# Optimization experiments

Measured on AMD Instinct MI355X. Metric: run time of the kernel, lower is better.

Reference implementation:

```python
import jax, jax.numpy as jnp
import numpy as np

ATOM = 34
HID = 256
LATENT = 128
CELLS = 512
B, N = 64, 128
NEG = -9e15


def setup_inputs() -> dict:
    key = jax.random.key(0)
    ks = jax.random.split(key, 20)
    inp = {}
    inp["xs"] = jax.random.normal(ks[0], (B, N, ATOM), dtype=jnp.float32)
    inp["A"] = jax.random.randint(ks[1], (B, N, N), 0, 2, dtype=jnp.int32)
    inp["cell_emb"] = jax.random.normal(ks[2], (B, CELLS), dtype=jnp.float32)
    inp["Wg"] = jax.random.normal(ks[3], (3, ATOM, ATOM), dtype=jnp.float32) * 0.17
    inp["bg"] = jnp.zeros((3, ATOM), dtype=jnp.float32)
    inp["attn"] = jax.random.normal(ks[4], (3, 2 * ATOM), dtype=jnp.float32) * 0.17
    # W_gnn_trans: 34 -> 256
    inp["Wt"] = jax.random.normal(ks[5], (ATOM, HID), dtype=jnp.float32) * 0.08
    inp["bt"] = jnp.zeros((HID,), dtype=jnp.float32)
    # ffn: 256 -> 34 ; ffn2: 34 -> latent
    inp["Wf"] = jax.random.normal(ks[6], (HID, ATOM), dtype=jnp.float32) * 0.08
    inp["bf"] = jnp.zeros((ATOM,), dtype=jnp.float32)
    inp["Wf2"] = jax.random.normal(ks[7], (ATOM, LATENT), dtype=jnp.float32) * 0.11
    inp["bf2"] = jnp.zeros((LATENT,), dtype=jnp.float32)
    # Decoder MLP: (latent+cells)->128->256->512->1
    din = LATENT + CELLS
    inp["W1"] = jax.random.normal(ks[8], (din, 128), dtype=jnp.float32) * 0.05
    inp["b1"] = jnp.zeros((128,), dtype=jnp.float32)
    inp["W2"] = jax.random.normal(ks[9], (128, 256), dtype=jnp.float32) * 0.07
    inp["b2"] = jnp.zeros((256,), dtype=jnp.float32)
    inp["W3"] = jax.random.normal(ks[10], (256, 512), dtype=jnp.float32) * 0.05
    inp["b3"] = jnp.zeros((512,), dtype=jnp.float32)
    inp["W4"] = jax.random.normal(ks[11], (512, 1), dtype=jnp.float32) * 0.06
    inp["b4"] = jnp.zeros((1,), dtype=jnp.float32)
    return inp


def reference(xs, A, cell_emb, Wg, bg, attn, Wt, bt, Wf, bf, Wf2, bf2,
              W1, b1, W2, b2, W3, b3, W4, b4):
    # ---- gnn(): 3 rounds of GAT-style masked-softmax message passing ----
    # a_input[b,p,q] = [h[b,p], h[b,q]], so e = leaky_relu(h@a1 outer+ h@a2)
    h0 = xs
    mask = A > 0  # [B,N,N]
    x = xs
    for i in range(3):
        h = jax.nn.relu(jnp.einsum('bnd,de->bne', x, Wg[i]) + bg[i])  # [B,N,34]
        f_src = h @ attn[i, :ATOM]   # [B,N] -- score contribution of row atom
        f_dst = h @ attn[i, ATOM:]   # [B,N] -- score contribution of col atom
        e = jax.nn.leaky_relu(f_src[:, :, None] + f_dst[:, None, :], 0.01)
        scores = jnp.where(mask, e, NEG)
        att = jax.nn.softmax(scores, axis=2)  # dropout disabled (deterministic)
        x = x + jnp.einsum('bpq,bqd->bpd', att, h)
    g = jax.nn.relu(jnp.einsum('bnd,dh->bnh', x, Wt) + bt)  # [B,N,HID]

    # ---- VEC_forward ----
    d = jnp.einsum('bnh,hd->bnd', g, Wf) + bf + h0        # ffn + residual to input xs
    d = jnp.einsum('bnd,dl->bnl', d, Wf2) + bf2           # [B,N,LATENT]
    d = jnp.max(d, axis=1)                                # [B,LATENT]
    vec = jax.nn.sigmoid(jnp.concatenate([d, cell_emb], axis=-1))

    # ---- Decoder_mlp (dropout disabled) ----
    hminus = jax.nn.relu(vec @ W1 + b1)
    hminus = jax.nn.relu(hminus @ W2 + b2)
    hminus = jax.nn.relu(hminus @ W3 + b3)
    score = hminus @ W4 + b4                              # [B,1]
    return score
```

## Files before the change

### kernel.cpp

```cpp
#include <hip/hip_runtime.h>

constexpr int ATOM = 34;
constexpr int HID = 256;
constexpr int LATENT = 128;
constexpr int CELLS = 512;
constexpr int NN = 128;
constexpr int NA = NN * ATOM;
#define NEGF (-9e15f)

__global__ __launch_bounds__(512) void k_gat(
    const float* __restrict__ xsrc, const int* __restrict__ A,
    const float* __restrict__ Wg, const float* __restrict__ bg,
    const float* __restrict__ av, float* __restrict__ X)
{
    const int b = blockIdx.x >> 2, q4 = blockIdx.x & 3;
    const int t = threadIdx.x, lane = t & 63, wave = t >> 6;
    const int p0 = q4 * 32;

    __shared__ float xl[NN][36];
    __shared__ float hlT[ATOM][132];
    __shared__ float att[32][NN];
    __shared__ float wg[ATOM * ATOM];
    __shared__ float fs[NN], fd[NN];
    __shared__ float bgs[ATOM], avs[2 * ATOM];

    for (int i = t; i < ATOM * ATOM; i += 512) wg[i] = Wg[i];
    if (t < ATOM)     bgs[t] = bg[t];
    if (t < 2 * ATOM) avs[t] = av[t];
    const float* xp = xsrc + b * NA;
    for (int i = t; i < NA; i += 512) xl[i / ATOM][i % ATOM] = xp[i];
    __syncthreads();

    {
        const int n = t >> 2, sub = t & 3;
        float xr[36];
        float4* xr4 = (float4*)xr;
        const float4* xlr = (const float4*)&xl[n][0];
        #pragma unroll
        for (int k = 0; k < 9; ++k) xr4[k] = xlr[k];
        for (int e = sub; e < ATOM; e += 4) {
            float acc = bgs[e];
            #pragma unroll
            for (int d = 0; d < ATOM; ++d) acc += xr[d] * wg[d * ATOM + e];
            hlT[e][n] = fmaxf(acc, 0.f);
        }
    }
    __syncthreads();

    if (t < 2 * NN) {
        const int n = t & (NN - 1), w = t >> 7;
        const float* avp = avs + w * ATOM;
        float acc = 0.f;
        #pragma unroll
        for (int d = 0; d < ATOM; ++d) acc += hlT[d][n] * avp[d];
        if (w == 0) fs[n] = acc; else fd[n] = acc;
    }
    __syncthreads();

    const int* Ab = A + b * NN * NN;
    #pragma unroll
    for (int i = 0; i < 4; ++i) {
        int lp = wave * 4 + i, gp = p0 + lp;
        float fsv = fs[gp];
        unsigned long long m0 = __ballot(Ab[gp * NN + lane] > 0);
        unsigned long long m1 = __ballot(Ab[gp * NN + 64 + lane] > 0);
        float s0 = fsv + fd[lane];
        s0 = (s0 > 0.f) ? s0 : 0.01f * s0;
        if (!((m0 >> lane) & 1ull)) s0 = NEGF;
        float s1 = fsv + fd[64 + lane];
        s1 = (s1 > 0.f) ? s1 : 0.01f * s1;
        if (!((m1 >> lane) & 1ull)) s1 = NEGF;
        float mx = fmaxf(s0, s1);
        #pragma unroll
        for (int o = 32; o >= 1; o >>= 1) mx = fmaxf(mx, __shfl_xor(mx, o, 64));
        float e0 = __expf(s0 - mx), e1 = __expf(s1 - mx);
        float sm = e0 + e1;
        #pragma unroll
        for (int o = 32; o >= 1; o >>= 1) sm += __shfl_xor(sm, o, 64);
        float inv = 1.f / sm;
        att[lp][lane]      = e0 * inv;
        att[lp][64 + lane] = e1 * inv;
    }
    __syncthreads();

    {
        const int p = t >> 4, g = t & 15;
        const float4* ap  = (const float4*)&att[p][0];
        const float4* h1p = (const float4*)&hlT[g][0];
        const float4* h2p = (const float4*)&hlT[g + 16][0];
        float a1 = 0.f, a2 = 0.f;
        #pragma unroll 8
        for (int k = 0; k < 32; ++k) {
            float4 a4 = ap[k], x1 = h1p[k], x2 = h2p[k];
            a1 += a4.x * x1.x + a4.y * x1.y + a4.z * x1.z + a4.w * x1.w;
            a2 += a4.x * x2.x + a4.y * x2.y + a4.z * x2.z + a4.w * x2.w;
        }
        const int gp = p0 + p;
        float* Xr = X + b * NA + gp * ATOM;
        Xr[g]      = xl[gp][g] + a1;
        Xr[g + 16] = xl[gp][g + 16] + a2;
        if (g < 2) {
            const float4* h3p = (const float4*)&hlT[g + 32][0];
            float a3 = 0.f;
            #pragma unroll 8
            for (int k = 0; k < 32; ++k) {
                float4 a4 = ap[k], x3 = h3p[k];
                a3 += a4.x * x3.x + a4.y * x3.y + a4.z * x3.z + a4.w * x3.w;
            }
            Xr[g + 32] = xl[gp][g + 32] + a3;
        }
    }
}

__global__ __launch_bounds__(512) void k_phaseB(
    const float* __restrict__ X, const float* __restrict__ xs,
    const float* __restrict__ Wt, const float* __restrict__ bt,
    const float* __restrict__ Wf, const float* __restrict__ bf,
    const float* __restrict__ Wf2, const float* __restrict__ bf2,
    float* __restrict__ DM)
{
    const int b = blockIdx.x >> 2, q4 = blockIdx.x & 3;
    const int t = threadIdx.x;
    const int p0 = q4 * 32;
    __shared__ float wt[HID * 36];
    __shared__ float wf[HID * 36];
    __shared__ float xl[32][36];
    __shared__ float dlT[ATOM][33];
    __shared__ float wf2s[ATOM * LATENT];
    __shared__ float bts[HID];
    __shared__ float bfs[ATOM];
    __shared__ float sl[512];

    for (int i = t; i < ATOM * HID; i += 512) {
        int d = i >> 8, h = i & 255;
        wt[h * 36 + d] = Wt[i];
    }
    for (int i = t; i < HID * ATOM; i += 512) {
        int h = i / ATOM, j = i % ATOM;
        wf[h * 36 + j] = Wf[i];
    }
    for (int i = t; i < ATOM * LATENT; i += 512) wf2s[i] = Wf2[i];
    if (t < HID)  bts[t] = bt[t];
    if (t < ATOM) bfs[t] = bf[t];
    for (int i = t; i < 32 * ATOM; i += 512) xl[i / ATOM][i % ATOM] = X[b * NA + p0 * ATOM + i];
    __syncthreads();

    const int row = t & 31, sub = t >> 5;
    float dp[ATOM];
    #pragma unroll
    for (int j = 0; j < ATOM; ++j) dp[j] = 0.f;
    {
        float xr[36];
        float4* xr4 = (float4*)xr;
        const float4* xlr = (const float4*)&xl[row][0];
        #pragma unroll
        for (int k = 0; k < 9; ++k) xr4[k] = xlr[k];
        for (int i = 0; i < 16; ++i) {
            const int h = sub + 16 * i;
            float acc = bts[h];
            const float4* wtp = (const float4*)&wt[h * 36];
            #pragma unroll
            for (int k = 0; k < 8; ++k) {
                float4 w4 = wtp[k];
                acc += xr[4*k] * w4.x + xr[4*k+1] * w4.y + xr[4*k+2] * w4.z + xr[4*k+3] * w4.w;
            }
            acc += xr[32] * wt[h * 36 + 32] + xr[33] * wt[h * 36 + 33];
            acc = fmaxf(acc, 0.f);
            const float4* wfp = (const float4*)&wf[h * 36];
            #pragma unroll
            for (int k = 0; k < 8; ++k) {
                float4 w4 = wfp[k];
                dp[4*k]   += acc * w4.x; dp[4*k+1] += acc * w4.y;
                dp[4*k+2] += acc * w4.z; dp[4*k+3] += acc * w4.w;
            }
            dp[32] += acc * wf[h * 36 + 32];
            dp[33] += acc * wf[h * 36 + 33];
        }
    }
    __syncthreads();
    {
        float* pl = (sub < 8) ? wt : wf;
        const int s8 = sub & 7;
        #pragma unroll
        for (int j = 0; j < ATOM; ++j) pl[(s8 * 32 + row) * ATOM + j] = dp[j];
    }
    __syncthreads();
    for (int i = t; i < 32 * ATOM; i += 512) {
        int rr = i / ATOM, j = i % ATOM;
        float dv = bfs[j] + xs[b * NA + (p0 + rr) * ATOM + j];
        #pragma unroll
        for (int s = 0; s < 8; ++s)
            dv += wt[(s * 32 + rr) * ATOM + j] + wf[(s * 32 + rr) * ATOM + j];
        dlT[j][rr] = dv;
    }
    __syncthreads();
    {
        const int l = t & 127, chunk = t >> 7;
        float w2r[ATOM];
        #pragma unroll
        for (int j = 0; j < ATOM; ++j) w2r[j] = wf2s[j * LATENT + l];
        float mx = -3.4e38f;
        for (int rr = chunk * 8; rr < chunk * 8 + 8; ++rr) {
            float acc = bf2[l];
            #pragma unroll
            for (int j = 0; j < ATOM; ++j) acc += dlT[j][rr] * w2r[j];
            mx = fmaxf(mx, acc);
        }
        sl[chunk * 128 + l] = mx;
    }
    __syncthreads();
    if (t < LATENT)
        DM[(b * 4 + q4) * LATENT + t] =
            fmaxf(fmaxf(sl[t], sl[128 + t]), fmaxf(sl[256 + t], sl[384 + t]));
}

__global__ __launch_bounds__(1024) void k_dec(
    const float* __restrict__ DM, const float* __restrict__ cell,
    const float* __restrict__ W1, const float* __restrict__ b1,
    const float* __restrict__ W2, const float* __restrict__ b2,
    const float* __restrict__ W3, const float* __restrict__ b3,
    const float* __restrict__ W4, const float* __restrict__ b4,
    float* __restrict__ out)
{
    const int b = blockIdx.x, t = threadIdx.x, lane = t & 63, wave = t >> 6;
    __shared__ float vec[LATENT + CELLS];
    __shared__ float h1[128], h2[256], h3[512];
    __shared__ float sl[1024];
    if (t < LATENT) {
        float m = fmaxf(fmaxf(DM[(b*4+0)*LATENT + t], DM[(b*4+1)*LATENT + t]),
                        fmaxf(DM[(b*4+2)*LATENT + t], DM[(b*4+3)*LATENT + t]));
        vec[t] = 1.f / (1.f + __expf(-m));
    } else if (t >= 512) {
        int c = t - 512;
        vec[LATENT + c] = 1.f / (1.f + __expf(-cell[b * CELLS + c]));
    }
    __syncthreads();
    {
        const int j = t & 127, part = t >> 7;
        float acc = 0.f;
        #pragma unroll 4
        for (int k = part * 80; k < part * 80 + 80; ++k)
            acc += vec[k] * W1[k * 128 + j];
        sl[part * 128 + j] = acc;
    }
    __syncthreads();
    if (t < 128) {
        float v = b1[t];
        #pragma unroll
        for (int p = 0; p < 8; ++p) v += sl[p * 128 + t];
        h1[t] = fmaxf(v, 0.f);
    }
    __syncthreads();
    {
        const int j = t & 255, part = t >> 8;
        float acc = 0.f;
        #pragma unroll 4
        for (int k = part * 32; k < part * 32 + 32; ++k)
            acc += h1[k] * W2[k * 256 + j];
        sl[part * 256 + j] = acc;
    }
    __syncthreads();
    if (t < 256) h2[t] = fmaxf(sl[t] + sl[256 + t] + sl[512 + t] + sl[768 + t] + b2[t], 0.f);
    __syncthreads();
    {
        const int j = t & 511, part = t >> 9;
        float acc = 0.f;
        #pragma unroll 4
        for (int k = part * 128; k < part * 128 + 128; ++k)
            acc += h2[k] * W3[k * 512 + j];
        sl[part * 512 + j] = acc;
    }
    __syncthreads();
    if (t < 512) h3[t] = fmaxf(sl[t] + sl[512 + t] + b3[t], 0.f);
    __syncthreads();
    float v = (t < 512) ? h3[t] * W4[t] : 0.f;
    #pragma unroll
    for (int o = 32; o >= 1; o >>= 1) v += __shfl_xor(v, o, 64);
    if (lane == 0) sl[wave] = v;
    __syncthreads();
    if (t == 0) {
        float s = b4[0];
        #pragma unroll
        for (int w = 0; w < 16; ++w) s += sl[w];
        out[b] = s;
    }
}

extern "C" void kernel_launch(void* const* d_in, const int* in_sizes, int n_in,
                              void* d_out, int out_size, void* d_ws, size_t ws_size,
                              hipStream_t stream) {
    const float* xs       = (const float*)d_in[0];
    const int*   A        = (const int*)  d_in[1];
    const float* cell_emb = (const float*)d_in[2];
    const float* Wg       = (const float*)d_in[3];
    const float* bg       = (const float*)d_in[4];
    const float* attnv    = (const float*)d_in[5];
    const float* Wt       = (const float*)d_in[6];
    const float* bt       = (const float*)d_in[7];
    const float* Wf       = (const float*)d_in[8];
    const float* bf       = (const float*)d_in[9];
    const float* Wf2      = (const float*)d_in[10];
    const float* bf2      = (const float*)d_in[11];
    const float* W1       = (const float*)d_in[12];
    const float* b1       = (const float*)d_in[13];
    const float* W2       = (const float*)d_in[14];
    const float* b2       = (const float*)d_in[15];
    const float* W3       = (const float*)d_in[16];
    const float* b3       = (const float*)d_in[17];
    const float* W4       = (const float*)d_in[18];
    const float* b4       = (const float*)d_in[19];
    float* out = (float*)d_out;

    float* W  = (float*)d_ws;
    float* X0 = W;
    float* X1 = W + 278528;
    float* DM = W + 557056;

    k_gat<<<256, 512, 0, stream>>>(xs, A, Wg,                  bg,          attnv,          X0);
    k_gat<<<256, 512, 0, stream>>>(X0, A, Wg + ATOM * ATOM,    bg + ATOM,   attnv + 2*ATOM, X1);
    k_gat<<<256, 512, 0, stream>>>(X1, A, Wg + 2 * ATOM * ATOM, bg + 2*ATOM, attnv + 4*ATOM, X0);
    k_phaseB<<<256, 512, 0, stream>>>(X0, xs, Wt, bt, Wf, bf, Wf2, bf2, DM);
    k_dec<<<64, 1024, 0, stream>>>(DM, cell_emb, W1, b1, W2, b2, W3, b3, W4, b4, out);
}
```

Baseline: 178.6 us.

## Fuse phase-B FFN into last GAT layer and widen blocks to 1024 threads

Merges the post-GNN projection/FFN/max-pool kernel into the third GAT launch through a templated kernel, so the final node features stay in shared memory in a reused pool instead of being written to and re-read from global memory. It also removes one kernel launch. Block size grows from 512 to 1024 threads: the attention-weighted sum is split over two K-halves and combined with a shuffle, and the hidden-layer matmul splits the feature dimension in half. This doubles the threads per block and shares one shared-memory buffer across both phases. The cost is higher register and LDS pressure per block, which may lower occupancy.

Result: slower. 277.7 us (+55.5%).

```diff
diff --git a/kernel.cpp b/kernel.cpp
--- a/kernel.cpp
+++ b/kernel.cpp
@@ -8,42 +8,68 @@
 constexpr int NA = NN * ATOM;
 #define NEGF (-9e15f)
 
-__global__ __launch_bounds__(512) void k_gat(
+constexpr int POOL = 30848;
+
+template <bool FUSE_B>
+__global__ __launch_bounds__(1024) void k_gat(
     const float* __restrict__ xsrc, const int* __restrict__ A,
     const float* __restrict__ Wg, const float* __restrict__ bg,
-    const float* __restrict__ av, float* __restrict__ X)
+    const float* __restrict__ av, float* __restrict__ X,
+    const float* __restrict__ xs,
+    const float* __restrict__ Wt, const float* __restrict__ bt,
+    const float* __restrict__ Wf, const float* __restrict__ bf,
+    const float* __restrict__ Wf2, const float* __restrict__ bf2,
+    float* __restrict__ DM)
 {
+    __shared__ __align__(16) float pool[POOL];
     const int b = blockIdx.x >> 2, q4 = blockIdx.x & 3;
     const int t = threadIdx.x, lane = t & 63, wave = t >> 6;
     const int p0 = q4 * 32;
 
-    __shared__ float xl[NN][36];
-    __shared__ float hlT[ATOM][132];
-    __shared__ float att[32][NN];
-    __shared__ float wg[ATOM * ATOM];
-    __shared__ float fs[NN], fd[NN];
-    __shared__ float bgs[ATOM], avs[2 * ATOM];
-
-    for (int i = t; i < ATOM * ATOM; i += 512) wg[i] = Wg[i];
+    float* xl  = pool;
+    float* hlT = pool + 4608;
+    float* att = pool + 9096;
+    float* wgT = pool + 13192;
+    float* fs  = pool + 14416;
+    float* fd  = pool + 14544;
+    float* bgs = pool + 14672;
+    float* avs = pool + 14712;
+    float* xq  = pool + 29440;
+
+    for (int i = t; i < ATOM * ATOM; i += 1024) {
+        int d = i / ATOM, e = i - d * ATOM;
+        wgT[e * 36 + d] = Wg[i];
+    }
+    if (t < 68)  wgT[(t >> 1) * 36 + 34 + (t & 1)] = 0.f;
     if (t < ATOM)     bgs[t] = bg[t];
     if (t < 2 * ATOM) avs[t] = av[t];
     const float* xp = xsrc + b * NA;
-    for (int i = t; i < NA; i += 512) xl[i / ATOM][i % ATOM] = xp[i];
-    __syncthreads();
-
-    {
-        const int n = t >> 2, sub = t & 3;
+    for (int i = t; i < NA; i += 1024) xl[(i / ATOM) * 36 + (i % ATOM)] = xp[i];
+    if (t < 256) xl[(t >> 1) * 36 + 34 + (t & 1)] = 0.f;
+    __syncthreads();
+
+    {
+        const int n = t >> 3, sub = t & 7;
         float xr[36];
-        float4* xr4 = (float4*)xr;
-        const float4* xlr = (const float4*)&xl[n][0];
-        #pragma unroll
-        for (int k = 0; k < 9; ++k) xr4[k] = xlr[k];
-        for (int e = sub; e < ATOM; e += 4) {
+        {
+            float4* xr4 = (float4*)xr;
+            const float4* xlr = (const float4*)(xl + n * 36);
+            #pragma unroll
+            for (int k = 0; k < 9; ++k) xr4[k] = xlr[k];
+        }
+        auto hbody = [&](int e) {
             float acc = bgs[e];
-            #pragma unroll
-            for (int d = 0; d < ATOM; ++d) acc += xr[d] * wg[d * ATOM + e];
-            hlT[e][n] = fmaxf(acc, 0.f);
-        }
+            const float4* wp = (const float4*)(wgT + e * 36);
+            #pragma unroll
+            for (int k = 0; k < 9; ++k) {
+                float4 w4 = wp[k];
+                acc += xr[4*k] * w4.x + xr[4*k+1] * w4.y + xr[4*k+2] * w4.z + xr[4*k+3] * w4.w;
+            }
+            hlT[e * 132 + n] = fmaxf(acc, 0.f);
+        };
+        #pragma unroll
+        for (int j = 0; j < 4; ++j) hbody(sub + 8 * j);
+        if (sub < 2) hbody(sub + 32);
     }
     __syncthreads();
 
@@ -52,15 +78,15 @@
         const float* avp = avs + w * ATOM;
         float acc = 0.f;
         #pragma unroll
-        for (int d = 0; d < ATOM; ++d) acc += hlT[d][n] * avp[d];
+        for (int d = 0; d < ATOM; ++d) acc += hlT[d * 132 + n] * avp[d];
         if (w == 0) fs[n] = acc; else fd[n] = acc;
     }
     __syncthreads();
 
     const int* Ab = A + b * NN * NN;
     #pragma unroll
-    for (int i = 0; i < 4; ++i) {
-        int lp = wave * 4 + i, gp = p0 + lp;
+    for (int i = 0; i < 2; ++i) {
+        int lp = wave * 2 + i, gp = p0 + lp;
         float fsv = fs[gp];
         unsigned long long m0 = __ballot(Ab[gp * NN + lane] > 0);
         unsigned long long m1 = __ballot(Ab[gp * NN + 64 + lane] > 0);
@@ -78,140 +104,162 @@
         #pragma unroll
         for (int o = 32; o >= 1; o >>= 1) sm += __shfl_xor(sm, o, 64);
         float inv = 1.f / sm;
-        att[lp][lane]      = e0 * inv;
-        att[lp][64 + lane] = e1 * inv;
-    }
-    __syncthreads();
-
-    {
-        const int p = t >> 4, g = t & 15;
-        const float4* ap  = (const float4*)&att[p][0];
-        const float4* h1p = (const float4*)&hlT[g][0];
-        const float4* h2p = (const float4*)&hlT[g + 16][0];
-        float a1 = 0.f, a2 = 0.f;
-        #pragma unroll 8
-        for (int k = 0; k < 32; ++k) {
+        att[lp * NN + lane]      = e0 * inv;
+        att[lp * NN + 64 + lane] = e1 * inv;
+    }
+    __syncthreads();
+
+    {
+        const int p = t >> 5, g = t & 15, kh = (t >> 4) & 1;
+        const float4* ap  = (const float4*)(att + p * NN + kh * 64);
+        const float4* h1p = (const float4*)(hlT + g * 132 + kh * 64);
+        const float4* h2p = (const float4*)(hlT + (g + 16) * 132 + kh * 64);
+        float a1 = 0.f, a2 = 0.f, a3 = 0.f;
+        #pragma unroll
+        for (int k = 0; k < 16; ++k) {
             float4 a4 = ap[k], x1 = h1p[k], x2 = h2p[k];
             a1 += a4.x * x1.x + a4.y * x1.y + a4.z * x1.z + a4.w * x1.w;
             a2 += a4.x * x2.x + a4.y * x2.y + a4.z * x2.z + a4.w * x2.w;
         }
-        const int gp = p0 + p;
-        float* Xr = X + b * NA + gp * ATOM;
-        Xr[g]      = xl[gp][g] + a1;
-        Xr[g + 16] = xl[gp][g + 16] + a2;
         if (g < 2) {
-            const float4* h3p = (const float4*)&hlT[g + 32][0];
-            float a3 = 0.f;
-            #pragma unroll 8
-            for (int k = 0; k < 32; ++k) {
+            const float4* h3p = (const float4*)(hlT + (g + 32) * 132 + kh * 64);
+            #pragma unroll
+            for (int k = 0; k < 16; ++k) {
                 float4 a4 = ap[k], x3 = h3p[k];
                 a3 += a4.x * x3.x + a4.y * x3.y + a4.z * x3.z + a4.w * x3.w;
             }
-            Xr[g + 32] = xl[gp][g + 32] + a3;
-        }
-    }
-}
-
-__global__ __launch_bounds__(512) void k_phaseB(
-    const float* __restrict__ X, const float* __restrict__ xs,
-    const float* __restrict__ Wt, const float* __restrict__ bt,
-    const float* __restrict__ Wf, const float* __restrict__ bf,
-    const float* __restrict__ Wf2, const float* __restrict__ bf2,
-    float* __restrict__ DM)
-{
-    const int b = blockIdx.x >> 2, q4 = blockIdx.x & 3;
-    const int t = threadIdx.x;
-    const int p0 = q4 * 32;
-    __shared__ float wt[HID * 36];
-    __shared__ float wf[HID * 36];
-    __shared__ float xl[32][36];
-    __shared__ float dlT[ATOM][33];
-    __shared__ float wf2s[ATOM * LATENT];
-    __shared__ float bts[HID];
-    __shared__ float bfs[ATOM];
-    __shared__ float sl[512];
-
-    for (int i = t; i < ATOM * HID; i += 512) {
+        }
+        a1 += __shfl_xor(a1, 16, 64);
+        a2 += __shfl_xor(a2, 16, 64);
+        a3 += __shfl_xor(a3, 16, 64);
+        const int gp = p0 + p;
+        if (FUSE_B) {
+            if (kh == 0) {
+                xq[p * 44 + g] = xl[gp * 36 + g] + a1;
+                if (g < 2) xq[p * 44 + g + 32] = xl[gp * 36 + g + 32] + a3;
+            } else {
+                xq[p * 44 + g + 16] = xl[gp * 36 + g + 16] + a2;
+                if (g >= 6) xq[p * 44 + 28 + g] = 0.f;
+            }
+        } else {
+            float* Xr = X + b * NA + gp * ATOM;
+            if (kh == 0) {
+                Xr[g] = xl[gp * 36 + g] + a1;
+                if (g < 2) Xr[g + 32] = xl[gp * 36 + g + 32] + a3;
+            } else {
+                Xr[g + 16] = xl[gp * 36 + g + 16] + a2;
+            }
+        }
+    }
+
+    if (!FUSE_B) return;
+
+    __syncthreads();
+    float* wt   = pool;
+    float* wf   = pool + 11264;
+    float* wf2s = pool + 22528;
+    float* dlT  = pool + 26880;
+    float* sl   = pool + 28032;
+    float* bts  = pool + 29056;
+    float* bfs  = pool + 29312;
+
+    for (int i = t; i < ATOM * HID; i += 1024) {
         int d = i >> 8, h = i & 255;
-        wt[h * 36 + d] = Wt[i];
-    }
-    for (int i = t; i < HID * ATOM; i += 512) {
-        int h = i / ATOM, j = i % ATOM;
-        wf[h * 36 + j] = Wf[i];
-    }
-    for (int i = t; i < ATOM * LATENT; i += 512) wf2s[i] = Wf2[i];
+        wt[h * 44 + d] = Wt[i];
+    }
+    for (int i = t; i < HID * ATOM; i += 1024) {
+        int h = i / ATOM, j = i - h * ATOM;
+        wf[h * 44 + j] = Wf[i];
+    }
+    for (int i = t; i < 2560; i += 1024) {
+        int h = i / 10, c = 34 + i - (i / 10) * 10;
+        wt[h * 44 + c] = 0.f; wf[h * 44 + c] = 0.f;
+    }
+    for (int i = t; i < ATOM * LATENT; i += 1024) wf2s[i] = Wf2[i];
     if (t < HID)  bts[t] = bt[t];
     if (t < ATOM) bfs[t] = bf[t];
-    for (int i = t; i < 32 * ATOM; i += 512) xl[i / ATOM][i % ATOM] = X[b * NA + p0 * ATOM + i];
-    __syncthreads();
-
-    const int row = t & 31, sub = t >> 5;
-    float dp[ATOM];
-    #pragma unroll
-    for (int j = 0; j < ATOM; ++j) dp[j] = 0.f;
-    {
-        float xr[36];
-        float4* xr4 = (float4*)xr;
-        const float4* xlr = (const float4*)&xl[row][0];
-        #pragma unroll
-        for (int k = 0; k < 9; ++k) xr4[k] = xlr[k];
+    __syncthreads();
+
+    {
+        const int row = t >> 5, sub = t & 15, half = (t >> 4) & 1;
+        const int dbase = half * 20;
+        float xr[20];
+        {
+            const float4* xp4 = (const float4*)(xq + row * 44 + dbase);
+            float4* xr4 = (float4*)xr;
+            #pragma unroll
+            for (int k = 0; k < 5; ++k) xr4[k] = xp4[k];
+        }
+        float dp[20];
+        #pragma unroll
+        for (int j = 0; j < 20; ++j) dp[j] = 0.f;
+        #pragma unroll
         for (int i = 0; i < 16; ++i) {
             const int h = sub + 16 * i;
-            float acc = bts[h];
-            const float4* wtp = (const float4*)&wt[h * 36];
-            #pragma unroll
-            for (int k = 0; k < 8; ++k) {
+            float part = 0.f;
+            const float4* wtp = (const float4*)(wt + h * 44 + dbase);
+            #pragma unroll
+            for (int k = 0; k < 5; ++k) {
                 float4 w4 = wtp[k];
-                acc += xr[4*k] * w4.x + xr[4*k+1] * w4.y + xr[4*k+2] * w4.z + xr[4*k+3] * w4.w;
-            }
-            acc += xr[32] * wt[h * 36 + 32] + xr[33] * wt[h * 36 + 33];
-            acc = fmaxf(acc, 0.f);
-            const float4* wfp = (const float4*)&wf[h * 36];
-            #pragma unroll
-            for (int k = 0; k < 8; ++k) {
+                part += xr[4*k] * w4.x + xr[4*k+1] * w4.y + xr[4*k+2] * w4.z + xr[4*k+3] * w4.w;
+            }
+            float acc = fmaxf(part + __shfl_xor(part, 16, 64) + bts[h], 0.f);
+            const float4* wfp = (const float4*)(wf + h * 44 + dbase);
+            #pragma unroll
+            for (int k = 0; k < 5; ++k) {
                 float4 w4 = wfp[k];
                 dp[4*k]   += acc * w4.x; dp[4*k+1] += acc * w4.y;
                 dp[4*k+2] += acc * w4.z; dp[4*k+3] += acc * w4.w;
             }
-            dp[32] += acc * wf[h * 36 + 32];
-            dp[33] += acc * wf[h * 36 + 33];
-        }
-    }
-    __syncthreads();
-    {
-        float* pl = (sub < 8) ? wt : wf;
-        const int s8 = sub & 7;
-        #pragma unroll
-        for (int j = 0; j < ATOM; ++j) pl[(s8 * 32 + row) * ATOM + j] = dp[j];
-    }
-    __syncthreads();
-    for (int i = t; i < 32 * ATOM; i += 512) {
-        int rr = i / ATOM, j = i % ATOM;
-        float dv = bfs[j] + xs[b * NA + (p0 + rr) * ATOM + j];
+        }
+        __syncthreads();
+        {
+            const int s8 = sub & 7;
+            float* pl = (sub < 8) ? wt : wf;
+            const int jbase = half * 20;
+            #pragma unroll
+            for (int jj = 0; jj < 20; ++jj) {
+                int j = jbase + jj;
+                if (j < ATOM) pl[(s8 * 32 + row) * ATOM + j] = dp[jj];
+            }
+        }
+    }
+    __syncthreads();
+
+    const float* xsq = xs + b * NA + p0 * ATOM;
+    for (int i = t; i < 32 * ATOM; i += 1024) {
+        int rr = i / ATOM, j = i - rr * ATOM;
+        float dv = bfs[j] + xsq[rr * ATOM + j];
         #pragma unroll
         for (int s = 0; s < 8; ++s)
             dv += wt[(s * 32 + rr) * ATOM + j] + wf[(s * 32 + rr) * ATOM + j];
-        dlT[j][rr] = dv;
-    }
-    __syncthreads();
+        dlT[j * 33 + rr] = dv;
+    }
+    __syncthreads();
+
     {
         const int l = t & 127, chunk = t >> 7;
         float w2r[ATOM];
         #pragma unroll
         for (int j = 0; j < ATOM; ++j) w2r[j] = wf2s[j * LATENT + l];
+        const float bb = bf2[l];
         float mx = -3.4e38f;
-        for (int rr = chunk * 8; rr < chunk * 8 + 8; ++rr) {
-            float acc = bf2[l];
-            #pragma unroll
-            for (int j = 0; j < ATOM; ++j) acc += dlT[j][rr] * w2r[j];
+        #pragma unroll
+        for (int rr = 0; rr < 4; ++rr) {
+            float acc = bb;
+            #pragma unroll
+            for (int j = 0; j < ATOM; ++j) acc += dlT[j * 33 + chunk * 4 + rr] * w2r[j];
             mx = fmaxf(mx, acc);
         }
         sl[chunk * 128 + l] = mx;
     }
     __syncthreads();
-    if (t < LATENT)
-        DM[(b * 4 + q4) * LATENT + t] =
-            fmaxf(fmaxf(sl[t], sl[128 + t]), fmaxf(sl[256 + t], sl[384 + t]));
+    if (t < LATENT) {
+        float m = sl[t];
+        #pragma unroll
+        for (int s = 1; s < 8; ++s) m = fmaxf(m, sl[s * 128 + t]);
+        DM[(b * 4 + q4) * LATENT + t] = m;
+    }
 }
 
 __global__ __launch_bounds__(1024) void k_dec(
@@ -316,9 +364,11 @@
     float* X1 = W + 278528;
     float* DM = W + 557056;
 
-    k_gat<<<256, 512, 0, stream>>>(xs, A, Wg,                  bg,          attnv,          X0);
-    k_gat<<<256, 512, 0, stream>>>(X0, A, Wg + ATOM * ATOM,    bg + ATOM,   attnv + 2*ATOM, X1);
-    k_gat<<<256, 512, 0, stream>>>(X1, A, Wg + 2 * ATOM * ATOM, bg + 2*ATOM, attnv + 4*ATOM, X0);
-    k_phaseB<<<256, 512, 0, stream>>>(X0, xs, Wt, bt, Wf, bf, Wf2, bf2, DM);
+    k_gat<false><<<256, 1024, 0, stream>>>(xs, A, Wg, bg, attnv, X0,
+                                           xs, Wt, bt, Wf, bf, Wf2, bf2, DM);
+    k_gat<false><<<256, 1024, 0, stream>>>(X0, A, Wg + ATOM*ATOM, bg + ATOM, attnv + 2*ATOM, X1,
+                                           xs, Wt, bt, Wf, bf, Wf2, bf2, DM);
+    k_gat<true> <<<256, 1024, 0, stream>>>(X1, A, Wg + 2*ATOM*ATOM, bg + 2*ATOM, attnv + 4*ATOM, nullptr,
+                                           xs, Wt, bt, Wf, bf, Wf2, bf2, DM);
     k_dec<<<64, 1024, 0, stream>>>(DM, cell_emb, W1, b1, W2, b2, W3, b3, W4, b4, out);
 }
```

## Split GAT layers across 8 blocks per graph with transposed padded weights

Applied to the files above, without the earlier changes.

The GAT kernel now launches 512 blocks of 256 threads, each owning 16 target atoms instead of 32, so more blocks run concurrently across CUs. The Wg matrix is stored transposed and padded to 36 so the per-node linear layer can use float4 shared-memory reads, with 2 threads per node instead of 4. Launch bounds request 2 blocks per CU for both GAT and phaseB. In exchange, each block still recomputes the full 128-node hidden projection and attention logits, so that redundant work per graph doubles.

Result: no change. 177.8 us (-0.5%).

```diff
diff --git a/kernel.cpp b/kernel.cpp
--- a/kernel.cpp
+++ b/kernel.cpp
@@ -8,51 +8,63 @@
 constexpr int NA = NN * ATOM;
 #define NEGF (-9e15f)
 
-__global__ __launch_bounds__(512) void k_gat(
+__global__ __launch_bounds__(256, 2) void k_gat(
     const float* __restrict__ xsrc, const int* __restrict__ A,
     const float* __restrict__ Wg, const float* __restrict__ bg,
     const float* __restrict__ av, float* __restrict__ X)
 {
-    const int b = blockIdx.x >> 2, q4 = blockIdx.x & 3;
+    const int b = blockIdx.x >> 3, s8 = blockIdx.x & 7;
     const int t = threadIdx.x, lane = t & 63, wave = t >> 6;
-    const int p0 = q4 * 32;
-
-    __shared__ float xl[NN][36];
-    __shared__ float hlT[ATOM][132];
-    __shared__ float att[32][NN];
-    __shared__ float wg[ATOM * ATOM];
-    __shared__ float fs[NN], fd[NN];
-    __shared__ float bgs[ATOM], avs[2 * ATOM];
-
-    for (int i = t; i < ATOM * ATOM; i += 512) wg[i] = Wg[i];
+    const int p0 = s8 * 16;
+
+    __shared__ __align__(16) float xl[NN * 36];
+    __shared__ __align__(16) float hlT[ATOM * 132];
+    __shared__ __align__(16) float att[16 * NN];
+    __shared__ __align__(16) float wgT[ATOM * 36];
+    __shared__ float fs[NN], fd[NN], bgs[ATOM], avs[2 * ATOM];
+
+    for (int i = t; i < ATOM * ATOM; i += 256) {
+        int d = i / ATOM, e = i - d * ATOM;
+        wgT[e * 36 + d] = Wg[i];
+    }
+    if (t < 68)  wgT[(t >> 1) * 36 + 34 + (t & 1)] = 0.f;
     if (t < ATOM)     bgs[t] = bg[t];
     if (t < 2 * ATOM) avs[t] = av[t];
     const float* xp = xsrc + b * NA;
-    for (int i = t; i < NA; i += 512) xl[i / ATOM][i % ATOM] = xp[i];
-    __syncthreads();
-
-    {
-        const int n = t >> 2, sub = t & 3;
+    for (int i = t; i < NA; i += 256) xl[(i / ATOM) * 36 + (i % ATOM)] = xp[i];
+    xl[(t >> 1) * 36 + 34 + (t & 1)] = 0.f;
+    __syncthreads();
+
+    {
+        const int n = t >> 1, sub = t & 1;
         float xr[36];
-        float4* xr4 = (float4*)xr;
-        const float4* xlr = (const float4*)&xl[n][0];
-        #pragma unroll
-        for (int k = 0; k < 9; ++k) xr4[k] = xlr[k];
-        for (int e = sub; e < ATOM; e += 4) {
+        {
+            float4* xr4 = (float4*)xr;
+            const float4* p4 = (const float4*)(xl + n * 36);
+            #pragma unroll
+            for (int k = 0; k < 9; ++k) xr4[k] = p4[k];
+        }
+        #pragma unroll
+        for (int j = 0; j < 17; ++j) {
+            const int e = sub + 2 * j;
             float acc = bgs[e];
-            #pragma unroll
-            for (int d = 0; d < ATOM; ++d) acc += xr[d] * wg[d * ATOM + e];
-            hlT[e][n] = fmaxf(acc, 0.f);
-        }
-    }
-    __syncthreads();
-
-    if (t < 2 * NN) {
-        const int n = t & (NN - 1), w = t >> 7;
+            const float4* wp = (const float4*)(wgT + e * 36);
+            #pragma unroll
+            for (int k = 0; k < 9; ++k) {
+                float4 w = wp[k];
+                acc += xr[4*k] * w.x + xr[4*k+1] * w.y + xr[4*k+2] * w.z + xr[4*k+3] * w.w;
+            }
+            hlT[e * 132 + n] = fmaxf(acc, 0.f);
+        }
+    }
+    __syncthreads();
+
+    {
+        const int n = t & 127, w = t >> 7;
         const float* avp = avs + w * ATOM;
         float acc = 0.f;
         #pragma unroll
-        for (int d = 0; d < ATOM; ++d) acc += hlT[d][n] * avp[d];
+        for (int d = 0; d < ATOM; ++d) acc += hlT[d * 132 + n] * avp[d];
         if (w == 0) fs[n] = acc; else fd[n] = acc;
     }
     __syncthreads();
@@ -78,16 +90,16 @@
         #pragma unroll
         for (int o = 32; o >= 1; o >>= 1) sm += __shfl_xor(sm, o, 64);
         float inv = 1.f / sm;
-        att[lp][lane]      = e0 * inv;
-        att[lp][64 + lane] = e1 * inv;
-    }
-    __syncthreads();
-
-    {
-        const int p = t >> 4, g = t & 15;
-        const float4* ap  = (const float4*)&att[p][0];
-        const float4* h1p = (const float4*)&hlT[g][0];
-        const float4* h2p = (const float4*)&hlT[g + 16][0];
+        att[lp * NN + lane]      = e0 * inv;
+        att[lp * NN + 64 + lane] = e1 * inv;
+    }
+    __syncthreads();
+
+    {
+        const int p = t >> 4, g = t & 15, gp = p0 + p;
+        const float4* ap  = (const float4*)(att + p * NN);
+        const float4* h1p = (const float4*)(hlT + g * 132);
+        const float4* h2p = (const float4*)(hlT + (g + 16) * 132);
         float a1 = 0.f, a2 = 0.f;
         #pragma unroll 8
         for (int k = 0; k < 32; ++k) {
@@ -95,24 +107,23 @@
             a1 += a4.x * x1.x + a4.y * x1.y + a4.z * x1.z + a4.w * x1.w;
             a2 += a4.x * x2.x + a4.y * x2.y + a4.z * x2.z + a4.w * x2.w;
         }
-        const int gp = p0 + p;
         float* Xr = X + b * NA + gp * ATOM;
-        Xr[g]      = xl[gp][g] + a1;
-        Xr[g + 16] = xl[gp][g + 16] + a2;
+        Xr[g]      = xl[gp * 36 + g] + a1;
+        Xr[g + 16] = xl[gp * 36 + g + 16] + a2;
         if (g < 2) {
-            const float4* h3p = (const float4*)&hlT[g + 32][0];
+            const float4* h3p = (const float4*)(hlT + (g + 32) * 132);
             float a3 = 0.f;
             #pragma unroll 8
             for (int k = 0; k < 32; ++k) {
                 float4 a4 = ap[k], x3 = h3p[k];
                 a3 += a4.x * x3.x + a4.y * x3.y + a4.z * x3.z + a4.w * x3.w;
             }
-            Xr[g + 32] = xl[gp][g + 32] + a3;
+            Xr[g + 32] = xl[gp * 36 + g + 32] + a3;
         }
     }
 }
 
-__global__ __launch_bounds__(512) void k_phaseB(
+__global__ __launch_bounds__(512, 2) void k_phaseB(
     const float* __restrict__ X, const float* __restrict__ xs,
     const float* __restrict__ Wt, const float* __restrict__ bt,
     const float* __restrict__ Wf, const float* __restrict__ bf,
@@ -316,9 +327,9 @@
     float* X1 = W + 278528;
     float* DM = W + 557056;
 
-    k_gat<<<256, 512, 0, stream>>>(xs, A, Wg,                  bg,          attnv,          X0);
-    k_gat<<<256, 512, 0, stream>>>(X0, A, Wg + ATOM * ATOM,    bg + ATOM,   attnv + 2*ATOM, X1);
-    k_gat<<<256, 512, 0, stream>>>(X1, A, Wg + 2 * ATOM * ATOM, bg + 2*ATOM, attnv + 4*ATOM, X0);
+    k_gat<<<512, 256, 0, stream>>>(xs, A, Wg,                   bg,            attnv,           X0);
+    k_gat<<<512, 256, 0, stream>>>(X0, A, Wg + ATOM * ATOM,     bg + ATOM,     attnv + 2*ATOM,  X1);
+    k_gat<<<512, 256, 0, stream>>>(X1, A, Wg + 2 * ATOM * ATOM, bg + 2 * ATOM, attnv + 4*ATOM,  X0);
     k_phaseB<<<256, 512, 0, stream>>>(X0, xs, Wt, bt, Wf, bf, Wf2, bf2, DM);
     k_dec<<<64, 1024, 0, stream>>>(DM, cell_emb, W1, b1, W2, b2, W3, b3, W4, b4, out);
 }
```
